# Kernel tuning notes

Measured on AMD Instinct MI355X. Metric: run time of the kernel, lower is better.

The kernel has to match this reference:

```python
import jax, jax.numpy as jnp
import numpy as np

TEMPERATURE = 0.07
EPS = 1e-8  # torch CosineSimilarity eps default


def setup_inputs() -> dict:
    key = jax.random.key(0)
    k1, k2 = jax.random.split(key)
    N, D = 8192, 1024
    image_features = jax.random.normal(k1, (N, D), dtype=jnp.float32)
    text_features = jax.random.normal(k2, (N, D), dtype=jnp.float32)
    return {"image_features": image_features, "text_features": text_features}


def _normalize(x):
    # matches torch cosine similarity denominator clamp: norm >= eps
    n = jnp.sqrt(jnp.sum(x * x, axis=-1, keepdims=True))
    return x / jnp.maximum(n, EPS)


def reference(image_features, text_features):
    # cosine similarity via normalize + GEMM (same math as broadcasted NxNxD form)
    img_n = _normalize(image_features)  # [N, D]
    txt_n = _normalize(text_features)   # [N, D]
    logits = jnp.einsum('id,jd->ij', img_n, txt_n) / TEMPERATURE  # [N, N]

    N = logits.shape[0]
    labels = jnp.arange(N)
    # cross-entropy with labels = diagonal indices
    logp_i2t = jax.nn.log_softmax(logits, axis=-1)      # rows: image -> text
    logp_t2i = jax.nn.log_softmax(logits.T, axis=-1)    # rows: text -> image
    loss_i2t = -jnp.mean(logp_i2t[labels, labels])
    loss_t2i = -jnp.mean(logp_t2i[labels, labels])
    return (loss_i2t + loss_t2i) / 2
```

## Files before the change

### kernel.cpp

```cpp
#include <hip/hip_runtime.h>


#define BM 128
#define BN 128
#define BKB 128

typedef float floatx4 __attribute__((ext_vector_type(4)));
typedef int   intx4   __attribute__((ext_vector_type(4)));
typedef int   intx8   __attribute__((ext_vector_type(8)));

__device__ __forceinline__ void gload_lds16(const unsigned char* g, unsigned char* lds) {
    __builtin_amdgcn_global_load_lds(
        (const __attribute__((address_space(1))) void*)g,
        (__attribute__((address_space(3))) void*)lds,
        16, 0, 0);
}

__global__ __launch_bounds__(256)
void normalize_fp8(const float* __restrict__ img, const float* __restrict__ txt,
                   unsigned int* __restrict__ oimg, unsigned int* __restrict__ otxt,
                   float* __restrict__ sums, float* __restrict__ out, int N) {
    const int gi = blockIdx.x * 256 + threadIdx.x;
    if (gi < 2 * N) sums[gi] = 0.f;
    if (gi == 0) out[0] = 0.f;

    const int gw = blockIdx.x * 4 + (threadIdx.x >> 6);
    const int lane = threadIdx.x & 63;
    const float* in = (gw < N) ? img : txt;
    unsigned int* o = (gw < N) ? oimg : otxt;
    const int row = (gw < N) ? gw : gw - N;
    const float4* rp = (const float4*)(in + (size_t)row * 1024);

    float4 v[4];
    float ss = 0.f;
    #pragma unroll
    for (int j = 0; j < 4; ++j) {
        v[j] = rp[j * 64 + lane];
        ss += v[j].x * v[j].x + v[j].y * v[j].y + v[j].z * v[j].z + v[j].w * v[j].w;
    }
    #pragma unroll
    for (int o2 = 1; o2 < 64; o2 <<= 1) ss += __shfl_xor(ss, o2);
    const float inv = 16.0f / fmaxf(sqrtf(ss), 1e-8f);
    #pragma unroll
    for (int j = 0; j < 4; ++j) {
        int p = __builtin_amdgcn_cvt_pk_fp8_f32(v[j].x * inv, v[j].y * inv, 0, false);
        p = __builtin_amdgcn_cvt_pk_fp8_f32(v[j].z * inv, v[j].w * inv, p, true);
        const int d = j * 64 + lane;
        const int c = (d >> 2) & 7;
        const int pp = (c & 1) * 4 + (c >> 1);
        const int dp = (d & ~31) | (pp * 4 + (d & 3));
        o[(size_t)row * 256 + dp] = (unsigned int)p;
    }
}

__global__ __launch_bounds__(256)
void gemm_exp_kernel(const unsigned char* __restrict__ A,
                     const unsigned char* __restrict__ B,
                     float* __restrict__ rowsum, float* __restrict__ colsum,
                     float* __restrict__ diag, int K, float scale) {
    __shared__ unsigned char As[2 * BM * 64];
    __shared__ unsigned char Bs[2 * BN * 64];

    const int bm = blockIdx.x, bn = blockIdx.y;
    const int tid = threadIdx.x;
    const int lane = tid & 63;
    const int wave = tid >> 6;
    const int quad = lane >> 4;
    const int lanelo = lane & 15;
    const int wrow = (wave >> 1) * 64;
    const int wcol = (wave & 1) * 64;

    floatx4 acc[4][4] = {};

    const int c0 = wave * 128 + lane;
    const int c1 = c0 + 64;
    const int r0 = c0 >> 2, r1 = c1 >> 2;
    const int kg0 = ((c0 & 3) ^ ((r0 >> 1) & 3)) * 16;
    const int kg1 = ((c1 & 3) ^ ((r1 >> 1) & 3)) * 16;

    const unsigned char* pa0 = A + (size_t)bm * BM * K + (size_t)r0 * K + kg0;
    const unsigned char* pa1 = A + (size_t)bm * BM * K + (size_t)r1 * K + kg1;
    const unsigned char* pb0 = B + (size_t)bn * BN * K + (size_t)r0 * K + kg0;
    const unsigned char* pb1 = B + (size_t)bn * BN * K + (size_t)r1 * K + kg1;
    unsigned char* dA0 = As + c0 * 16;
    unsigned char* dA1 = As + c1 * 16;
    unsigned char* dB0 = Bs + c0 * 16;
    unsigned char* dB1 = Bs + c1 * 16;

    int aoff[4], boff[4];
    #pragma unroll
    for (int t = 0; t < 4; ++t) {
        const int Ra = wrow + t * 16 + lanelo;
        const int Rb = wcol + t * 16 + lanelo;
        aoff[t] = Ra * 64 + ((quad ^ ((Ra >> 1) & 3)) * 16);
        boff[t] = Rb * 64 + ((quad ^ ((Rb >> 1) & 3)) * 16);
    }

    for (int k0 = 0; k0 < K; k0 += BKB) {
        #pragma unroll
        for (int w = 0; w < 2; ++w) {
            gload_lds16(pa0 + w * 64, dA0 + w * 8192);
            gload_lds16(pa1 + w * 64, dA1 + w * 8192);
            gload_lds16(pb0 + w * 64, dB0 + w * 8192);
            gload_lds16(pb1 + w * 64, dB1 + w * 8192);
        }
        pa0 += BKB; pa1 += BKB; pb0 += BKB; pb1 += BKB;
        __syncthreads();

        intx8 af[4], bg[4];
        #pragma unroll
        for (int t = 0; t < 4; ++t) {
            const intx4 alo = *(const intx4*)(As + aoff[t]);
            const intx4 ahi = *(const intx4*)(As + 8192 + aoff[t]);
            af[t] = __builtin_shufflevector(alo, ahi, 0, 1, 2, 3, 4, 5, 6, 7);
            const intx4 blo = *(const intx4*)(Bs + boff[t]);
            const intx4 bhi = *(const intx4*)(Bs + 8192 + boff[t]);
            bg[t] = __builtin_shufflevector(blo, bhi, 0, 1, 2, 3, 4, 5, 6, 7);
        }

        #pragma unroll
        for (int tm = 0; tm < 4; ++tm)
            #pragma unroll
            for (int tn = 0; tn < 4; ++tn)
                acc[tm][tn] = __builtin_amdgcn_mfma_scale_f32_16x16x128_f8f6f4(
                    af[tm], bg[tn], acc[tm][tn],
                    0, 0,
                    0, 127,
                    0, 127);
        __syncthreads();
    }

    const int growb = bm * BM + wrow;
    const int gcolb = bn * BN + wcol;

    #pragma unroll
    for (int tm = 0; tm < 4; ++tm)
        #pragma unroll
        for (int tn = 0; tn < 4; ++tn)
            #pragma unroll
            for (int r = 0; r < 4; ++r) {
                const float l = acc[tm][tn][r] * scale;
                const int grow = growb + tm * 16 + quad * 4 + r;
                const int gcol = gcolb + tn * 16 + lanelo;
                if (grow == gcol) diag[grow] = l;
                acc[tm][tn][r] = __expf(l);
            }

    #pragma unroll
    for (int tm = 0; tm < 4; ++tm) {
        floatx4 rs = acc[tm][0] + acc[tm][1] + acc[tm][2] + acc[tm][3];
        #pragma unroll
        for (int r = 0; r < 4; ++r) {
            float v = rs[r];
            v += __shfl_xor(v, 1);
            v += __shfl_xor(v, 2);
            v += __shfl_xor(v, 4);
            v += __shfl_xor(v, 8);
            if (lanelo == 0)
                atomicAdd(&rowsum[growb + tm * 16 + quad * 4 + r], v);
        }
    }

    #pragma unroll
    for (int tn = 0; tn < 4; ++tn) {
        float cs = 0.f;
        #pragma unroll
        for (int tm = 0; tm < 4; ++tm)
            cs += acc[tm][tn][0] + acc[tm][tn][1] + acc[tm][tn][2] + acc[tm][tn][3];
        cs += __shfl_xor(cs, 16);
        cs += __shfl_xor(cs, 32);
        if (quad == 0)
            atomicAdd(&colsum[gcolb + tn * 16 + lanelo], cs);
    }
}

__global__ __launch_bounds__(256)
void final_reduce(const float* __restrict__ rowsum, const float* __restrict__ colsum,
                  const float* __restrict__ diag, float* __restrict__ out, int n) {
    const int i = blockIdx.x * 256 + threadIdx.x;
    const int t = threadIdx.x;
    float v = 0.5f * (logf(rowsum[i]) + logf(colsum[i])) - diag[i];
    #pragma unroll
    for (int o = 1; o < 64; o <<= 1) v += __shfl_xor(v, o);
    __shared__ float ws[4];
    if ((t & 63) == 0) ws[t >> 6] = v;
    __syncthreads();
    if (t == 0) atomicAdd(out, (ws[0] + ws[1] + ws[2] + ws[3]) / (float)n);
}

extern "C" void kernel_launch(void* const* d_in, const int* in_sizes, int n_in,
                              void* d_out, int out_size, void* d_ws, size_t ws_size,
                              hipStream_t stream) {
    const float* img = (const float*)d_in[0];
    const float* txt = (const float*)d_in[1];
    float* out = (float*)d_out;

    const int D = 1024;
    const int N = in_sizes[0] / D;

    unsigned char* imgq = (unsigned char*)d_ws;
    unsigned char* txtq = imgq + (size_t)N * D;
    float* rowsum = (float*)(txtq + (size_t)N * D);
    float* colsum = rowsum + N;
    float* diag = colsum + N;

    normalize_fp8<<<2 * N / 4, 256, 0, stream>>>(img, txt, (unsigned int*)imgq,
                                                 (unsigned int*)txtq, rowsum, out, N);

    dim3 grid(N / BM, N / BN);
    gemm_exp_kernel<<<grid, 256, 0, stream>>>(imgq, txtq, rowsum, colsum, diag,
                                              D, 1.0f / (256.0f * 0.07f));
    final_reduce<<<N / 256, 256, 0, stream>>>(rowsum, colsum, diag, out, N);
}
```

Measured before the change: 189.3 us.

## Fuse final reduction into GEMM, swizzle tile order, coalesce fp8 stores

Removes the separate final_reduce launch: the last GEMM block to finish, found with an atomic counter, computes the loss over the row sums, column sums and diagonal. The GEMM grid becomes 1D and is remapped into 8x8 tile groups to improve L2 reuse of the A and B panels. The normalize kernel now permutes fp8 words with a lane shuffle so global stores are contiguous, instead of scattering them. The cost is a serial tail in which one block reduces N elements alone, and the counter adds an extra fence and atomic per block.

```diff
diff --git a/kernel.cpp b/kernel.cpp
--- a/kernel.cpp
+++ b/kernel.cpp
@@ -19,10 +19,11 @@
 __global__ __launch_bounds__(256)
 void normalize_fp8(const float* __restrict__ img, const float* __restrict__ txt,
                    unsigned int* __restrict__ oimg, unsigned int* __restrict__ otxt,
-                   float* __restrict__ sums, float* __restrict__ out, int N) {
+                   float* __restrict__ sums, int* __restrict__ counter,
+                   float* __restrict__ out, int N) {
     const int gi = blockIdx.x * 256 + threadIdx.x;
     if (gi < 2 * N) sums[gi] = 0.f;
-    if (gi == 0) out[0] = 0.f;
+    if (gi == 0) { out[0] = 0.f; *counter = 0; }
 
     const int gw = blockIdx.x * 4 + (threadIdx.x >> 6);
     const int lane = threadIdx.x & 63;
@@ -41,15 +42,17 @@
     #pragma unroll
     for (int o2 = 1; o2 < 64; o2 <<= 1) ss += __shfl_xor(ss, o2);
     const float inv = 16.0f / fmaxf(sqrtf(ss), 1e-8f);
+
+    const int p8 = (lane >> 2) & 7;
+    const int csrc = ((p8 & 3) << 1) | (p8 >> 2);
+    const int src = (lane & 32) | (csrc << 2) | (lane & 3);
+
     #pragma unroll
     for (int j = 0; j < 4; ++j) {
         int p = __builtin_amdgcn_cvt_pk_fp8_f32(v[j].x * inv, v[j].y * inv, 0, false);
         p = __builtin_amdgcn_cvt_pk_fp8_f32(v[j].z * inv, v[j].w * inv, p, true);
-        const int d = j * 64 + lane;
-        const int c = (d >> 2) & 7;
-        const int pp = (c & 1) * 4 + (c >> 1);
-        const int dp = (d & ~31) | (pp * 4 + (d & 3));
-        o[(size_t)row * 256 + dp] = (unsigned int)p;
+        const int ps = __shfl(p, src);
+        o[(size_t)row * 256 + j * 64 + lane] = (unsigned int)ps;
     }
 }
 
@@ -57,11 +60,16 @@
 void gemm_exp_kernel(const unsigned char* __restrict__ A,
                      const unsigned char* __restrict__ B,
                      float* __restrict__ rowsum, float* __restrict__ colsum,
-                     float* __restrict__ diag, int K, float scale) {
+                     float* __restrict__ diag, int* __restrict__ counter,
+                     float* __restrict__ out, int N, int K, float scale) {
+    const int id = blockIdx.x;
+    const int group = id >> 6, local = id & 63;
+    const int bm = (group & 7) * 8 + (local & 7);
+    const int bn = (group >> 3) * 8 + (local >> 3);
+
     __shared__ unsigned char As[2 * BM * 64];
     __shared__ unsigned char Bs[2 * BN * 64];
 
-    const int bm = blockIdx.x, bn = blockIdx.y;
     const int tid = threadIdx.x;
     const int lane = tid & 63;
     const int wave = tid >> 6;
@@ -172,20 +180,30 @@
         if (quad == 0)
             atomicAdd(&colsum[gcolb + tn * 16 + lanelo], cs);
     }
-}
-
-__global__ __launch_bounds__(256)
-void final_reduce(const float* __restrict__ rowsum, const float* __restrict__ colsum,
-                  const float* __restrict__ diag, float* __restrict__ out, int n) {
-    const int i = blockIdx.x * 256 + threadIdx.x;
-    const int t = threadIdx.x;
-    float v = 0.5f * (logf(rowsum[i]) + logf(colsum[i])) - diag[i];
-    #pragma unroll
-    for (int o = 1; o < 64; o <<= 1) v += __shfl_xor(v, o);
+
+    __threadfence();
+    __shared__ int lastflag;
+    if (tid == 0) {
+        const int old = atomicAdd(counter, 1);
+        lastflag = (old == (int)gridDim.x - 1);
+    }
+    __syncthreads();
+    if (!lastflag) return;
+    __threadfence();
+
+    float a = 0.f;
+    for (int i = tid; i < N; i += 256) {
+        const float rs = __hip_atomic_load(&rowsum[i], __ATOMIC_RELAXED, __HIP_MEMORY_SCOPE_AGENT);
+        const float cs = __hip_atomic_load(&colsum[i], __ATOMIC_RELAXED, __HIP_MEMORY_SCOPE_AGENT);
+        const float dg = __hip_atomic_load(&diag[i], __ATOMIC_RELAXED, __HIP_MEMORY_SCOPE_AGENT);
+        a += 0.5f * (logf(rs) + logf(cs)) - dg;
+    }
+    #pragma unroll
+    for (int o = 1; o < 64; o <<= 1) a += __shfl_xor(a, o);
     __shared__ float ws[4];
-    if ((t & 63) == 0) ws[t >> 6] = v;
+    if ((tid & 63) == 0) ws[tid >> 6] = a;
     __syncthreads();
-    if (t == 0) atomicAdd(out, (ws[0] + ws[1] + ws[2] + ws[3]) / (float)n);
+    if (tid == 0) out[0] = (ws[0] + ws[1] + ws[2] + ws[3]) / (float)N;
 }
 
 extern "C" void kernel_launch(void* const* d_in, const int* in_sizes, int n_in,
@@ -203,12 +221,13 @@
     float* rowsum = (float*)(txtq + (size_t)N * D);
     float* colsum = rowsum + N;
     float* diag = colsum + N;
+    int* counter = (int*)(diag + N);
 
     normalize_fp8<<<2 * N / 4, 256, 0, stream>>>(img, txt, (unsigned int*)imgq,
-                                                 (unsigned int*)txtq, rowsum, out, N);
-
-    dim3 grid(N / BM, N / BN);
-    gemm_exp_kernel<<<grid, 256, 0, stream>>>(imgq, txtq, rowsum, colsum, diag,
-                                              D, 1.0f / (256.0f * 0.07f));
-    final_reduce<<<N / 256, 256, 0, stream>>>(rowsum, colsum, diag, out, N);
-}
+                                                 (unsigned int*)txtq, rowsum,
+                                                 counter, out, N);
+
+    gemm_exp_kernel<<<(N / BM) * (N / BN), 256, 0, stream>>>(
+        imgq, txtq, rowsum, colsum, diag, counter, out,
+        N, D, 1.0f / (256.0f * 0.07f));
+}
```

Result: slower. 411.2 us (+117.3%).
